# Optimization experiments

Measured on AMD Instinct MI355X. Metric: run time of the kernel, lower is better.

The kernel has to match this reference:

```python
import jax, jax.numpy as jnp
import numpy as np

S = 8          # nodes per subgraph (last node is the anchor)
B = 8192       # number of subgraphs in the batch
N = B * S      # total nodes
E_PER = S * S  # edges per subgraph (dense local connectivity)
DIN, DOUT = 512, 256
EPS = 1e-12


def _block_edges(key):
    # local src/dst in [0,S) per subgraph, offset to global node ids
    k1, k2 = jax.random.split(key)
    src = jax.random.randint(k1, (B, E_PER), 0, S)
    dst = jax.random.randint(k2, (B, E_PER), 0, S)
    off = (jnp.arange(B) * S)[:, None]
    return (src + off).reshape(-1), (dst + off).reshape(-1)


def setup_inputs() -> dict:
    key = jax.random.key(0)
    ks = jax.random.split(key, 10)
    pos_src, pos_dst = _block_edges(ks[0])
    neg_src, neg_dst = _block_edges(ks[1])
    return {
        "pos_x": jax.random.normal(ks[2], (N, DIN), jnp.float32),
        "neg_x": jax.random.normal(ks[3], (N, DIN), jnp.float32),
        "pos_src": pos_src, "pos_dst": pos_dst,
        "pos_w": jax.random.uniform(ks[4], (B * E_PER,), jnp.float32),
        "neg_src": neg_src, "neg_dst": neg_dst,
        "neg_w": jax.random.uniform(ks[5], (B * E_PER,), jnp.float32),
        "W_gcn": jax.random.normal(ks[6], (DIN, DOUT), jnp.float32) / np.sqrt(DIN),
        "b_gcn": jnp.zeros((DOUT,), jnp.float32),
        "prelu_a": jnp.float32(0.25),
        "W_bil": jax.random.normal(ks[7], (DOUT, DOUT), jnp.float32) / np.sqrt(DOUT),
        "b_bil": jnp.zeros((1,), jnp.float32),
    }


def _l2norm(x):
    return x / jnp.maximum(jnp.linalg.norm(x, axis=1, keepdims=True), EPS)


def _gcn_branch(x, src, dst, w, W_gcn, b_gcn, prelu_a):
    # GraphConv(norm='none') with edge weights: h = A_w (X W) + b
    xw = x @ W_gcn                                      # [N, DOUT]
    agg = jnp.zeros_like(xw).at[dst].add(w[:, None] * xw[src])
    h = agg + b_gcn
    h = jnp.where(h >= 0, h, prelu_a * h)               # PReLU (single param)
    h = h.reshape(B, S, -1)                             # fixed-size subgraphs
    pool = jnp.mean(h[:, :-1], axis=1)                  # mean over non-anchor nodes
    anchor = h[:, -1]                                   # last node per subgraph
    return _l2norm(pool), _l2norm(anchor)


def reference(pos_x, neg_x, pos_src, pos_dst, pos_w, neg_src, neg_dst, neg_w,
              W_gcn, b_gcn, prelu_a, W_bil, b_bil):
    pos_pool, anchor = _gcn_branch(pos_x, pos_src, pos_dst, pos_w, W_gcn, b_gcn, prelu_a)
    neg_pool, _ = _gcn_branch(neg_x, neg_src, neg_dst, neg_w, W_gcn, b_gcn, prelu_a)
    # Bilinear(D, D, 1): score_b = pool_b^T W anchor_b + bias
    pos_scores = jnp.einsum('bd,de,be->b', pos_pool, W_bil, anchor) + b_bil[0]
    neg_scores = jnp.einsum('bd,de,be->b', neg_pool, W_bil, anchor) + b_bil[0]
    return pos_scores, neg_scores
```

## Files before the change

### kernel.cpp

```cpp
#include <hip/hip_runtime.h>
#include <stdint.h>
#include <math.h>

#define SS 8
#define NBLK 8192
#define DIN 512
#define DOUT 256
#define GB 8
#define MT 64
#define BK 32
#define KSTEPS 16
#define VSTR 264
#define EPSN 1e-12f

typedef __bf16 bf16;
typedef __bf16 bf16x8 __attribute__((ext_vector_type(8)));
typedef float  f32x4  __attribute__((ext_vector_type(4)));

typedef __attribute__((address_space(3))) uint32_t       lds_u32;
typedef __attribute__((address_space(1))) const uint32_t g_u32;

__device__ __forceinline__ void dma16(const void* g, void* l) {
    __builtin_amdgcn_global_load_lds((g_u32*)g, (lds_u32*)l, 16, 0, 0);
}

__device__ __forceinline__ bf16x8 cvt8(f32x4 lo, f32x4 hi) {
    bf16x8 r;
    r[0] = (bf16)lo[0]; r[1] = (bf16)lo[1]; r[2] = (bf16)lo[2]; r[3] = (bf16)lo[3];
    r[4] = (bf16)hi[0]; r[5] = (bf16)hi[1]; r[6] = (bf16)hi[2]; r[7] = (bf16)hi[3];
    return r;
}

__global__ void prep_kernel(const float* __restrict__ W_gcn,
                            const float* __restrict__ W_bil,
                            bf16* __restrict__ Wt,
                            bf16* __restrict__ Wh,
                            bf16* __restrict__ Wl) {
    int idx = blockIdx.x * 256 + threadIdx.x;
    if (idx < DIN * DOUT) {
        int k = idx >> 8, n = idx & 255;
        Wt[((size_t)(k >> 5) * DOUT + n) * BK + (k & 31)] = (bf16)W_gcn[idx];
    } else {
        int j = idx - DIN * DOUT;
        float wv = W_bil[j];
        bf16 h = (bf16)wv;
        Wh[j] = h;
        Wl[j] = (bf16)(wv - (float)h);
    }
}

__global__ __launch_bounds__(256, 2) void cola_fused6(
    const float* __restrict__ pos_x, const float* __restrict__ neg_x,
    const int* __restrict__ pos_src, const int* __restrict__ pos_dst,
    const float* __restrict__ pos_w,
    const int* __restrict__ neg_src, const int* __restrict__ neg_dst,
    const float* __restrict__ neg_w,
    const bf16* __restrict__ Wt, const bf16* __restrict__ Wh,
    const bf16* __restrict__ Wl,
    const float* __restrict__ b_gcn, const float* __restrict__ prelu_a,
    const float* __restrict__ b_bil, float* __restrict__ out)
{
    __shared__ __align__(16) float bufA[3][2][MT * BK];
    __shared__ float adjP[GB][SS][SS];
    __shared__ float adjN[GB][SS][SS];
    __shared__ float red[5 * GB];

    float* pool_pos = (float*)&bufA[0][0][0];
    float* v_lds    = pool_pos + GB * DOUT;
    bf16*  ahs      = (bf16*)&bufA[1][0][0];
    bf16*  als      = ahs + GB * VSTR;

    const int t    = threadIdx.x;
    const int wg   = blockIdx.x;
    const int w    = t >> 6;
    const int lane = t & 63;
    const int q    = lane >> 4;
    const int r15  = lane & 15;
    const int row0 = wg * MT;

    for (int i = t; i < GB * 64; i += 256) { ((float*)adjP)[i] = 0.f; ((float*)adjN)[i] = 0.f; }
    if (t < 5 * GB) red[t] = 0.f;
    __syncthreads();

    {
        int2   sp2 = ((const int2*)pos_src)[wg * 256 + t];
        int2   dp2 = ((const int2*)pos_dst)[wg * 256 + t];
        float2 wp2 = ((const float2*)pos_w)[wg * 256 + t];
        int2   sn2 = ((const int2*)neg_src)[wg * 256 + t];
        int2   dn2 = ((const int2*)neg_dst)[wg * 256 + t];
        float2 wn2 = ((const float2*)neg_w)[wg * 256 + t];
        int gl = t >> 5;
        int base = (wg * GB + gl) * SS;
        atomicAdd(&adjP[gl][dp2.x - base][sp2.x - base], wp2.x);
        atomicAdd(&adjP[gl][dp2.y - base][sp2.y - base], wp2.y);
        atomicAdd(&adjN[gl][dn2.x - base][sn2.x - base], wn2.x);
        atomicAdd(&adjN[gl][dn2.y - base][sn2.y - base], wn2.y);
    }

    const int arow_off = lane >> 3;
    const int akq      = (lane & 7) ^ arow_off;

    auto issueA = [&](int s, int bufi) {
        const int kbase = s * BK;
#pragma unroll
        for (int h = 0; h < 2; ++h) {
            int c = w * 2 + h;
            int row = c * 8 + arow_off;
            dma16(pos_x + (size_t)(row0 + row) * DIN + kbase + akq * 4,
                  &bufA[bufi][0][c * 256]);
            dma16(neg_x + (size_t)(row0 + row) * DIN + kbase + akq * 4,
                  &bufA[bufi][1][c * 256]);
        }
    };

    auto loadB = [&](bf16x8* dst, int s) {
#pragma unroll
        for (int ni = 0; ni < 4; ++ni)
            dst[ni] = *(const bf16x8*)(Wt +
                ((size_t)s * DOUT + w * 64 + ni * 16 + r15) * BK + q * 8);
    };

    f32x4 accp[4][4], accn[4][4];
#pragma unroll
    for (int mi = 0; mi < 4; ++mi)
#pragma unroll
        for (int ni = 0; ni < 4; ++ni) {
            accp[mi][ni] = (f32x4){0.f, 0.f, 0.f, 0.f};
            accn[mi][ni] = (f32x4){0.f, 0.f, 0.f, 0.f};
        }

    bf16x8 breg[2][4];

    issueA(0, 0);
    loadB(breg[0], 0);
    issueA(1, 1);

#pragma unroll
    for (int s = 0; s < KSTEPS; ++s) {
        if (s == KSTEPS - 1)
            asm volatile("s_waitcnt vmcnt(0) lgkmcnt(0)" ::: "memory");
        else
            asm volatile("s_waitcnt vmcnt(4) lgkmcnt(0)" ::: "memory");
        __builtin_amdgcn_s_barrier();
        __builtin_amdgcn_sched_barrier(0);

        if (s + 1 < KSTEPS) loadB(breg[(s + 1) & 1], s + 1);
        if (s + 2 < KSTEPS) issueA(s + 2, (s + 2) % 3);

        const int bufi = s % 3;
        const bf16x8* bfv = breg[s & 1];
        const int q0 = (2 * q) ^ (r15 & 7);
        const int q1 = q0 ^ 1;
        bf16x8 afp[4], afn[4];
#pragma unroll
        for (int mi = 0; mi < 4; ++mi) {
            int m = mi * 16 + r15;
            f32x4 lo = *(const f32x4*)&bufA[bufi][0][m * BK + q0 * 4];
            f32x4 hi = *(const f32x4*)&bufA[bufi][0][m * BK + q1 * 4];
            afp[mi] = cvt8(lo, hi);
            lo = *(const f32x4*)&bufA[bufi][1][m * BK + q0 * 4];
            hi = *(const f32x4*)&bufA[bufi][1][m * BK + q1 * 4];
            afn[mi] = cvt8(lo, hi);
        }
#pragma unroll
        for (int mi = 0; mi < 4; ++mi)
#pragma unroll
            for (int ni = 0; ni < 4; ++ni) {
                accp[mi][ni] = __builtin_amdgcn_mfma_f32_16x16x32_bf16(
                    afp[mi], bfv[ni], accp[mi][ni], 0, 0, 0);
                accn[mi][ni] = __builtin_amdgcn_mfma_f32_16x16x32_bf16(
                    afn[mi], bfv[ni], accn[mi][ni], 0, 0, 0);
            }
    }
    __syncthreads();

    const float pa = *prelu_a;

#pragma unroll
    for (int mi = 0; mi < 4; ++mi) {
        const int gl = mi * 2 + (q >> 1);
        float part = 0.f;
#pragma unroll
        for (int ni = 0; ni < 4; ++ni) {
            float r0, r1, r2, r3, r4, r5, r6, r7;
#pragma unroll
            for (int r = 0; r < 4; ++r) {
                float own = accp[mi][ni][r];
                float oth = __shfl_xor(own, 16);
                float lo = ((q & 1) == 0) ? own : oth;
                float hi = ((q & 1) == 0) ? oth : own;
                if (r == 0) { r0 = lo; r4 = hi; }
                else if (r == 1) { r1 = lo; r5 = hi; }
                else if (r == 2) { r2 = lo; r6 = hi; }
                else            { r3 = lo; r7 = hi; }
            }
            int c = w * 64 + ni * 16 + r15;
            float bg = b_gcn[c];
            float pool = 0.f, anch = 0.f;
#pragma unroll
            for (int d = 0; d < 8; ++d) {
                const float* ar = &adjP[gl][d][0];
                float a = bg + ar[0]*r0 + ar[1]*r1 + ar[2]*r2 + ar[3]*r3
                             + ar[4]*r4 + ar[5]*r5 + ar[6]*r6 + ar[7]*r7;
                float h = (a >= 0.f) ? a : pa * a;
                if (d < 7) pool += h; else anch = h;
            }
            float pl = pool * (1.f / 7.f);
            if ((q & 1) == 0) {
                pool_pos[gl * DOUT + c] = pl;
                part += pl * pl;
            } else {
                bf16 hh = (bf16)anch;
                ahs[gl * VSTR + c] = hh;
                als[gl * VSTR + c] = (bf16)(anch - (float)hh);
                part += anch * anch;
            }
        }
        part += __shfl_xor(part, 8);
        part += __shfl_xor(part, 4);
        part += __shfl_xor(part, 2);
        part += __shfl_xor(part, 1);
        if (r15 == 0) atomicAdd((q & 1) ? &red[GB + gl] : &red[gl], part);
    }
    __syncthreads();

    {
        f32x4 accv[4];
#pragma unroll
        for (int ni = 0; ni < 4; ++ni) accv[ni] = (f32x4){0.f, 0.f, 0.f, 0.f};
        const int ga = (r15 & 7) * VSTR;
#pragma unroll
        for (int ks = 0; ks < 8; ++ks) {
            bf16x8 ah_f = *(const bf16x8*)(ahs + ga + ks * 32 + q * 8);
            bf16x8 al_f = *(const bf16x8*)(als + ga + ks * 32 + q * 8);
#pragma unroll
            for (int ni = 0; ni < 4; ++ni) {
                int d = w * 64 + ni * 16 + r15;
                bf16x8 bh = *(const bf16x8*)(Wh + (size_t)d * DOUT + ks * 32 + q * 8);
                bf16x8 bl = *(const bf16x8*)(Wl + (size_t)d * DOUT + ks * 32 + q * 8);
                accv[ni] = __builtin_amdgcn_mfma_f32_16x16x32_bf16(ah_f, bh, accv[ni], 0, 0, 0);
                accv[ni] = __builtin_amdgcn_mfma_f32_16x16x32_bf16(al_f, bh, accv[ni], 0, 0, 0);
                accv[ni] = __builtin_amdgcn_mfma_f32_16x16x32_bf16(ah_f, bl, accv[ni], 0, 0, 0);
            }
        }
        float sp[4] = {0.f, 0.f, 0.f, 0.f};
        if (q < 2) {
#pragma unroll
            for (int ni = 0; ni < 4; ++ni) {
                int c = w * 64 + ni * 16 + r15;
#pragma unroll
                for (int r = 0; r < 4; ++r) {
                    int g = q * 4 + r;
                    v_lds[g * DOUT + c] = accv[ni][r];
                    sp[r] += accv[ni][r] * pool_pos[g * DOUT + c];
                }
            }
        }
#pragma unroll
        for (int r = 0; r < 4; ++r) {
            sp[r] += __shfl_xor(sp[r], 8);
            sp[r] += __shfl_xor(sp[r], 4);
            sp[r] += __shfl_xor(sp[r], 2);
            sp[r] += __shfl_xor(sp[r], 1);
        }
        if (q < 2 && r15 == 0) {
#pragma unroll
            for (int r = 0; r < 4; ++r) atomicAdd(&red[3 * GB + q * 4 + r], sp[r]);
        }
    }
    __syncthreads();

#pragma unroll
    for (int mi = 0; mi < 4; ++mi) {
        const int gl = mi * 2 + (q >> 1);
        float part = 0.f;
#pragma unroll
        for (int ni = 0; ni < 4; ++ni) {
            float r0, r1, r2, r3, r4, r5, r6, r7;
#pragma unroll
            for (int r = 0; r < 4; ++r) {
                float own = accn[mi][ni][r];
                float oth = __shfl_xor(own, 16);
                float lo = ((q & 1) == 0) ? own : oth;
                float hi = ((q & 1) == 0) ? oth : own;
                if (r == 0) { r0 = lo; r4 = hi; }
                else if (r == 1) { r1 = lo; r5 = hi; }
                else if (r == 2) { r2 = lo; r6 = hi; }
                else            { r3 = lo; r7 = hi; }
            }
            int c = w * 64 + ni * 16 + r15;
            float bg = b_gcn[c];
            float pool = 0.f;
#pragma unroll
            for (int d = 0; d < 7; ++d) {
                const float* ar = &adjN[gl][d][0];
                float a = bg + ar[0]*r0 + ar[1]*r1 + ar[2]*r2 + ar[3]*r3
                             + ar[4]*r4 + ar[5]*r5 + ar[6]*r6 + ar[7]*r7;
                float h = (a >= 0.f) ? a : pa * a;
                pool += h;
            }
            float pl = pool * (1.f / 7.f);
            part += ((q & 1) == 0) ? pl * v_lds[gl * DOUT + c] : pl * pl;
        }
        part += __shfl_xor(part, 8);
        part += __shfl_xor(part, 4);
        part += __shfl_xor(part, 2);
        part += __shfl_xor(part, 1);
        if (r15 == 0) atomicAdd((q & 1) ? &red[2 * GB + gl] : &red[4 * GB + gl], part);
    }
    __syncthreads();

    if (t < GB) {
        float np = fmaxf(sqrtf(red[t]), EPSN);
        float na = fmaxf(sqrtf(red[GB + t]), EPSN);
        float nn = fmaxf(sqrtf(red[2 * GB + t]), EPSN);
        float bb = b_bil[0];
        out[wg * GB + t]        = red[3 * GB + t] / (np * na) + bb;
        out[NBLK + wg * GB + t] = red[4 * GB + t] / (nn * na) + bb;
    }
}

extern "C" void kernel_launch(void* const* d_in, const int* in_sizes, int n_in,
                              void* d_out, int out_size, void* d_ws, size_t ws_size,
                              hipStream_t stream) {
    const float* pos_x   = (const float*)d_in[0];
    const float* neg_x   = (const float*)d_in[1];
    const int*   pos_src = (const int*)d_in[2];
    const int*   pos_dst = (const int*)d_in[3];
    const float* pos_w   = (const float*)d_in[4];
    const int*   neg_src = (const int*)d_in[5];
    const int*   neg_dst = (const int*)d_in[6];
    const float* neg_w   = (const float*)d_in[7];
    const float* W_gcn   = (const float*)d_in[8];
    const float* b_gcn   = (const float*)d_in[9];
    const float* prelu_a = (const float*)d_in[10];
    const float* W_bil   = (const float*)d_in[11];
    const float* b_bil   = (const float*)d_in[12];
    float* outp = (float*)d_out;

    bf16* Wt = (bf16*)d_ws;
    bf16* Wh = Wt + DIN * DOUT;
    bf16* Wl = Wh + DOUT * DOUT;

    prep_kernel<<<(DIN * DOUT + DOUT * DOUT) / 256, 256, 0, stream>>>(W_gcn, W_bil, Wt, Wh, Wl);
    cola_fused6<<<NBLK / GB, 256, 0, stream>>>(
        pos_x, neg_x, pos_src, pos_dst, pos_w, neg_src, neg_dst, neg_w,
        Wt, Wh, Wl, b_gcn, prelu_a, b_bil, outp);
}
```

Baseline: 366.3 us.

## Split pos/neg GEMM branches across two wave groups in 512-thread blocks

Workgroups grow from 256 to 512 threads. Waves 0-3 compute the positive-branch GEMM and waves 4-7 the negative one, so each wave holds half as many accumulators. Launch bounds rise to 4 and the bilinear MFMA stage is spread over all 8 waves. This aims to lower register pressure and raise occupancy and latency hiding. The cost is that half the waves idle during each branch-specific epilogue, and every wave still loads its own copy of the B fragments.

```diff
diff --git a/kernel.cpp b/kernel.cpp
--- a/kernel.cpp
+++ b/kernel.cpp
@@ -49,7 +49,7 @@
     }
 }
 
-__global__ __launch_bounds__(256, 2) void cola_fused6(
+__global__ __launch_bounds__(512, 4) void cola_fused7(
     const float* __restrict__ pos_x, const float* __restrict__ neg_x,
     const int* __restrict__ pos_src, const int* __restrict__ pos_dst,
     const float* __restrict__ pos_w,
@@ -73,43 +73,42 @@
     const int t    = threadIdx.x;
     const int wg   = blockIdx.x;
     const int w    = t >> 6;
+    const int b    = w >> 2;
+    const int wq   = w & 3;
     const int lane = t & 63;
     const int q    = lane >> 4;
     const int r15  = lane & 15;
     const int row0 = wg * MT;
 
-    for (int i = t; i < GB * 64; i += 256) { ((float*)adjP)[i] = 0.f; ((float*)adjN)[i] = 0.f; }
+    for (int i = t; i < GB * 64; i += 512) { ((float*)adjP)[i] = 0.f; ((float*)adjN)[i] = 0.f; }
     if (t < 5 * GB) red[t] = 0.f;
     __syncthreads();
 
     {
-        int2   sp2 = ((const int2*)pos_src)[wg * 256 + t];
-        int2   dp2 = ((const int2*)pos_dst)[wg * 256 + t];
-        float2 wp2 = ((const float2*)pos_w)[wg * 256 + t];
-        int2   sn2 = ((const int2*)neg_src)[wg * 256 + t];
-        int2   dn2 = ((const int2*)neg_dst)[wg * 256 + t];
-        float2 wn2 = ((const float2*)neg_w)[wg * 256 + t];
-        int gl = t >> 5;
+        int   sp = pos_src[wg * 512 + t];
+        int   dp = pos_dst[wg * 512 + t];
+        float wp = pos_w[wg * 512 + t];
+        int   sn = neg_src[wg * 512 + t];
+        int   dn = neg_dst[wg * 512 + t];
+        float wn = neg_w[wg * 512 + t];
+        int gl = t >> 6;
         int base = (wg * GB + gl) * SS;
-        atomicAdd(&adjP[gl][dp2.x - base][sp2.x - base], wp2.x);
-        atomicAdd(&adjP[gl][dp2.y - base][sp2.y - base], wp2.y);
-        atomicAdd(&adjN[gl][dn2.x - base][sn2.x - base], wn2.x);
-        atomicAdd(&adjN[gl][dn2.y - base][sn2.y - base], wn2.y);
+        atomicAdd(&adjP[gl][dp - base][sp - base], wp);
+        atomicAdd(&adjN[gl][dn - base][sn - base], wn);
     }
 
     const int arow_off = lane >> 3;
     const int akq      = (lane & 7) ^ arow_off;
+    const float* xb    = (b == 0) ? pos_x : neg_x;
 
     auto issueA = [&](int s, int bufi) {
         const int kbase = s * BK;
 #pragma unroll
         for (int h = 0; h < 2; ++h) {
-            int c = w * 2 + h;
+            int c = wq * 2 + h;
             int row = c * 8 + arow_off;
-            dma16(pos_x + (size_t)(row0 + row) * DIN + kbase + akq * 4,
-                  &bufA[bufi][0][c * 256]);
-            dma16(neg_x + (size_t)(row0 + row) * DIN + kbase + akq * 4,
-                  &bufA[bufi][1][c * 256]);
+            dma16(xb + (size_t)(row0 + row) * DIN + kbase + akq * 4,
+                  &bufA[bufi][b][c * 256]);
         }
     };
 
@@ -117,17 +116,15 @@
 #pragma unroll
         for (int ni = 0; ni < 4; ++ni)
             dst[ni] = *(const bf16x8*)(Wt +
-                ((size_t)s * DOUT + w * 64 + ni * 16 + r15) * BK + q * 8);
+                ((size_t)s * DOUT + wq * 64 + ni * 16 + r15) * BK + q * 8);
     };
 
-    f32x4 accp[4][4], accn[4][4];
+    f32x4 acc[4][4];
 #pragma unroll
     for (int mi = 0; mi < 4; ++mi)
 #pragma unroll
-        for (int ni = 0; ni < 4; ++ni) {
-            accp[mi][ni] = (f32x4){0.f, 0.f, 0.f, 0.f};
-            accn[mi][ni] = (f32x4){0.f, 0.f, 0.f, 0.f};
-        }
+        for (int ni = 0; ni < 4; ++ni)
+            acc[mi][ni] = (f32x4){0.f, 0.f, 0.f, 0.f};
 
     bf16x8 breg[2][4];
 
@@ -140,7 +137,7 @@
         if (s == KSTEPS - 1)
             asm volatile("s_waitcnt vmcnt(0) lgkmcnt(0)" ::: "memory");
         else
-            asm volatile("s_waitcnt vmcnt(4) lgkmcnt(0)" ::: "memory");
+            asm volatile("s_waitcnt vmcnt(2) lgkmcnt(0)" ::: "memory");
         __builtin_amdgcn_s_barrier();
         __builtin_amdgcn_sched_barrier(0);
 
@@ -151,91 +148,87 @@
         const bf16x8* bfv = breg[s & 1];
         const int q0 = (2 * q) ^ (r15 & 7);
         const int q1 = q0 ^ 1;
-        bf16x8 afp[4], afn[4];
+        bf16x8 af[4];
 #pragma unroll
         for (int mi = 0; mi < 4; ++mi) {
             int m = mi * 16 + r15;
-            f32x4 lo = *(const f32x4*)&bufA[bufi][0][m * BK + q0 * 4];
-            f32x4 hi = *(const f32x4*)&bufA[bufi][0][m * BK + q1 * 4];
-            afp[mi] = cvt8(lo, hi);
-            lo = *(const f32x4*)&bufA[bufi][1][m * BK + q0 * 4];
-            hi = *(const f32x4*)&bufA[bufi][1][m * BK + q1 * 4];
-            afn[mi] = cvt8(lo, hi);
+            f32x4 lo = *(const f32x4*)&bufA[bufi][b][m * BK + q0 * 4];
+            f32x4 hi = *(const f32x4*)&bufA[bufi][b][m * BK + q1 * 4];
+            af[mi] = cvt8(lo, hi);
         }
 #pragma unroll
         for (int mi = 0; mi < 4; ++mi)
 #pragma unroll
+            for (int ni = 0; ni < 4; ++ni)
+                acc[mi][ni] = __builtin_amdgcn_mfma_f32_16x16x32_bf16(
+                    af[mi], bfv[ni], acc[mi][ni], 0, 0, 0);
+    }
+    __syncthreads();
+
+    const float pa = *prelu_a;
+
+    if (w < 4) {
+#pragma unroll
+        for (int mi = 0; mi < 4; ++mi) {
+            const int gl = mi * 2 + (q >> 1);
+            float part = 0.f;
+#pragma unroll
             for (int ni = 0; ni < 4; ++ni) {
-                accp[mi][ni] = __builtin_amdgcn_mfma_f32_16x16x32_bf16(
-                    afp[mi], bfv[ni], accp[mi][ni], 0, 0, 0);
-                accn[mi][ni] = __builtin_amdgcn_mfma_f32_16x16x32_bf16(
-                    afn[mi], bfv[ni], accn[mi][ni], 0, 0, 0);
+                float r0, r1, r2, r3, r4, r5, r6, r7;
+#pragma unroll
+                for (int r = 0; r < 4; ++r) {
+                    float own = acc[mi][ni][r];
+                    float oth = __shfl_xor(own, 16);
+                    float lo = ((q & 1) == 0) ? own : oth;
+                    float hi = ((q & 1) == 0) ? oth : own;
+                    if (r == 0) { r0 = lo; r4 = hi; }
+                    else if (r == 1) { r1 = lo; r5 = hi; }
+                    else if (r == 2) { r2 = lo; r6 = hi; }
+                    else            { r3 = lo; r7 = hi; }
+                }
+                int c = wq * 64 + ni * 16 + r15;
+                float bg = b_gcn[c];
+                float pool = 0.f, anch = 0.f;
+#pragma unroll
+                for (int d = 0; d < 8; ++d) {
+                    const float* ar = &adjP[gl][d][0];
+                    float a = bg + ar[0]*r0 + ar[1]*r1 + ar[2]*r2 + ar[3]*r3
+                                 + ar[4]*r4 + ar[5]*r5 + ar[6]*r6 + ar[7]*r7;
+                    float h = (a >= 0.f) ? a : pa * a;
+                    if (d < 7) pool += h; else anch = h;
+                }
+                float pl = pool * (1.f / 7.f);
+                if ((q & 1) == 0) {
+                    pool_pos[gl * DOUT + c] = pl;
+                    part += pl * pl;
+                } else {
+                    bf16 hh = (bf16)anch;
+                    ahs[gl * VSTR + c] = hh;
+                    als[gl * VSTR + c] = (bf16)(anch - (float)hh);
+                    part += anch * anch;
+                }
             }
-    }
-    __syncthreads();
-
-    const float pa = *prelu_a;
-
-#pragma unroll
-    for (int mi = 0; mi < 4; ++mi) {
-        const int gl = mi * 2 + (q >> 1);
-        float part = 0.f;
-#pragma unroll
-        for (int ni = 0; ni < 4; ++ni) {
-            float r0, r1, r2, r3, r4, r5, r6, r7;
-#pragma unroll
-            for (int r = 0; r < 4; ++r) {
-                float own = accp[mi][ni][r];
-                float oth = __shfl_xor(own, 16);
-                float lo = ((q & 1) == 0) ? own : oth;
-                float hi = ((q & 1) == 0) ? oth : own;
-                if (r == 0) { r0 = lo; r4 = hi; }
-                else if (r == 1) { r1 = lo; r5 = hi; }
-                else if (r == 2) { r2 = lo; r6 = hi; }
-                else            { r3 = lo; r7 = hi; }
-            }
-            int c = w * 64 + ni * 16 + r15;
-            float bg = b_gcn[c];
-            float pool = 0.f, anch = 0.f;
-#pragma unroll
-            for (int d = 0; d < 8; ++d) {
-                const float* ar = &adjP[gl][d][0];
-                float a = bg + ar[0]*r0 + ar[1]*r1 + ar[2]*r2 + ar[3]*r3
-                             + ar[4]*r4 + ar[5]*r5 + ar[6]*r6 + ar[7]*r7;
-                float h = (a >= 0.f) ? a : pa * a;
-                if (d < 7) pool += h; else anch = h;
-            }
-            float pl = pool * (1.f / 7.f);
-            if ((q & 1) == 0) {
-                pool_pos[gl * DOUT + c] = pl;
-                part += pl * pl;
-            } else {
-                bf16 hh = (bf16)anch;
-                ahs[gl * VSTR + c] = hh;
-                als[gl * VSTR + c] = (bf16)(anch - (float)hh);
-                part += anch * anch;
-            }
-        }
-        part += __shfl_xor(part, 8);
-        part += __shfl_xor(part, 4);
-        part += __shfl_xor(part, 2);
-        part += __shfl_xor(part, 1);
-        if (r15 == 0) atomicAdd((q & 1) ? &red[GB + gl] : &red[gl], part);
+            part += __shfl_xor(part, 8);
+            part += __shfl_xor(part, 4);
+            part += __shfl_xor(part, 2);
+            part += __shfl_xor(part, 1);
+            if (r15 == 0) atomicAdd((q & 1) ? &red[GB + gl] : &red[gl], part);
+        }
     }
     __syncthreads();
 
     {
-        f32x4 accv[4];
-#pragma unroll
-        for (int ni = 0; ni < 4; ++ni) accv[ni] = (f32x4){0.f, 0.f, 0.f, 0.f};
+        f32x4 accv[2];
+        accv[0] = (f32x4){0.f, 0.f, 0.f, 0.f};
+        accv[1] = (f32x4){0.f, 0.f, 0.f, 0.f};
         const int ga = (r15 & 7) * VSTR;
 #pragma unroll
         for (int ks = 0; ks < 8; ++ks) {
             bf16x8 ah_f = *(const bf16x8*)(ahs + ga + ks * 32 + q * 8);
             bf16x8 al_f = *(const bf16x8*)(als + ga + ks * 32 + q * 8);
 #pragma unroll
-            for (int ni = 0; ni < 4; ++ni) {
-                int d = w * 64 + ni * 16 + r15;
+            for (int ni = 0; ni < 2; ++ni) {
+                int d = w * 32 + ni * 16 + r15;
                 bf16x8 bh = *(const bf16x8*)(Wh + (size_t)d * DOUT + ks * 32 + q * 8);
                 bf16x8 bl = *(const bf16x8*)(Wl + (size_t)d * DOUT + ks * 32 + q * 8);
                 accv[ni] = __builtin_amdgcn_mfma_f32_16x16x32_bf16(ah_f, bh, accv[ni], 0, 0, 0);
@@ -246,8 +239,8 @@
         float sp[4] = {0.f, 0.f, 0.f, 0.f};
         if (q < 2) {
 #pragma unroll
-            for (int ni = 0; ni < 4; ++ni) {
-                int c = w * 64 + ni * 16 + r15;
+            for (int ni = 0; ni < 2; ++ni) {
+                int c = w * 32 + ni * 16 + r15;
 #pragma unroll
                 for (int r = 0; r < 4; ++r) {
                     int g = q * 4 + r;
@@ -270,43 +263,45 @@
     }
     __syncthreads();
 
-#pragma unroll
-    for (int mi = 0; mi < 4; ++mi) {
-        const int gl = mi * 2 + (q >> 1);
-        float part = 0.f;
-#pragma unroll
-        for (int ni = 0; ni < 4; ++ni) {
-            float r0, r1, r2, r3, r4, r5, r6, r7;
-#pragma unroll
-            for (int r = 0; r < 4; ++r) {
-                float own = accn[mi][ni][r];
-                float oth = __shfl_xor(own, 16);
-                float lo = ((q & 1) == 0) ? own : oth;
-                float hi = ((q & 1) == 0) ? oth : own;
-                if (r == 0) { r0 = lo; r4 = hi; }
-                else if (r == 1) { r1 = lo; r5 = hi; }
-                else if (r == 2) { r2 = lo; r6 = hi; }
-                else            { r3 = lo; r7 = hi; }
+    if (w >= 4) {
+#pragma unroll
+        for (int mi = 0; mi < 4; ++mi) {
+            const int gl = mi * 2 + (q >> 1);
+            float part = 0.f;
+#pragma unroll
+            for (int ni = 0; ni < 4; ++ni) {
+                float r0, r1, r2, r3, r4, r5, r6, r7;
+#pragma unroll
+                for (int r = 0; r < 4; ++r) {
+                    float own = acc[mi][ni][r];
+                    float oth = __shfl_xor(own, 16);
+                    float lo = ((q & 1) == 0) ? own : oth;
+                    float hi = ((q & 1) == 0) ? oth : own;
+                    if (r == 0) { r0 = lo; r4 = hi; }
+                    else if (r == 1) { r1 = lo; r5 = hi; }
+                    else if (r == 2) { r2 = lo; r6 = hi; }
+                    else            { r3 = lo; r7 = hi; }
+                }
+                int c = wq * 64 + ni * 16 + r15;
+                float bg = b_gcn[c];
+                float pool = 0.f;
+#pragma unroll
+                for (int d = 0; d < 7; ++d) {
+                    const float* ar = &adjN[gl][d][0];
+                    float a = bg + ar[0]*r0 + ar[1]*r1 + ar[2]*r2 + ar[3]*r3
+                                 + ar[4]*r4 + ar[5]*r5 + ar[6]*r6 + ar[7]*r7;
+                    float h = (a >= 0.f) ? a : pa * a;
+                    pool += h;
+                }
+                float pl = pool * (1.f / 7.f);
+                part += ((q & 1) == 0) ? pl * v_lds[gl * DOUT + c] : pl * pl;
             }
-            int c = w * 64 + ni * 16 + r15;
-            float bg = b_gcn[c];
-            float pool = 0.f;
-#pragma unroll
-            for (int d = 0; d < 7; ++d) {
-                const float* ar = &adjN[gl][d][0];
-                float a = bg + ar[0]*r0 + ar[1]*r1 + ar[2]*r2 + ar[3]*r3
-                             + ar[4]*r4 + ar[5]*r5 + ar[6]*r6 + ar[7]*r7;
-                float h = (a >= 0.f) ? a : pa * a;
-                pool += h;
-            }
-            float pl = pool * (1.f / 7.f);
-            part += ((q & 1) == 0) ? pl * v_lds[gl * DOUT + c] : pl * pl;
-        }
-        part += __shfl_xor(part, 8);
-        part += __shfl_xor(part, 4);
-        part += __shfl_xor(part, 2);
-        part += __shfl_xor(part, 1);
-        if (r15 == 0) atomicAdd((q & 1) ? &red[2 * GB + gl] : &red[4 * GB + gl], part);
+            part += __shfl_xor(part, 8);
+            part += __shfl_xor(part, 4);
+            part += __shfl_xor(part, 2);
+            part += __shfl_xor(part, 1);
+            if (r15 == 0) atomicAdd((q & 1) ? &red[2 * GB + gl] : &red[4 * GB + gl], part);
+        }
     }
     __syncthreads();
 
@@ -343,7 +338,7 @@
     bf16* Wl = Wh + DOUT * DOUT;
 
     prep_kernel<<<(DIN * DOUT + DOUT * DOUT) / 256, 256, 0, stream>>>(W_gcn, W_bil, Wt, Wh, Wl);
-    cola_fused6<<<NBLK / GB, 256, 0, stream>>>(
+    cola_fused7<<<NBLK / GB, 512, 0, stream>>>(
         pos_x, neg_x, pos_src, pos_dst, pos_w, neg_src, neg_dst, neg_w,
         Wt, Wh, Wl, b_gcn, prelu_a, b_bil, outp);
 }
```

Result: slower. 396.6 us (+8.3%).
